# Performance work log

Measured on AMD Instinct MI355X. Metric: run time of the kernel, lower is better.

The kernel has to match this reference:

```python
import jax, jax.numpy as jnp
import numpy as np

BATCH, SEQ, DIM, NH = 4, 2048, 1024, 16
HD = DIM // NH  # 64

def _rope_cos_sin(seq_len, head_dim, dtype=jnp.float32):
    inv_freq = 1.0 / (10000.0 ** (jnp.arange(0, head_dim, 2, dtype=dtype) / head_dim))
    t = jnp.arange(seq_len, dtype=dtype)
    freqs = jnp.outer(t, inv_freq)                # (seq, hd/2)
    emb = jnp.concatenate([freqs, freqs], axis=-1)  # (seq, hd)
    return jnp.cos(emb), jnp.sin(emb)

def _apply_rope(x, cos, sin):
    # x: (b, h, s, d); cos/sin: (s, d)
    d2 = x.shape[-1] // 2
    x1, x2 = x[..., :d2], x[..., d2:]
    c = cos[None, None, :, :d2]
    s = sin[None, None, :, :d2]
    return jnp.concatenate([x1 * c - x2 * s, x1 * s + x2 * c], axis=-1)

def setup_inputs() -> dict:
    key = jax.random.key(0)
    ks = jax.random.split(key, 3)
    x = jax.random.normal(ks[0], (BATCH, SEQ, DIM), dtype=jnp.float32)
    Wqkv = jax.random.normal(ks[1], (DIM, 3 * DIM), dtype=jnp.float32) * (1.0 / np.sqrt(DIM))
    bqkv = jnp.zeros((3 * DIM,), dtype=jnp.float32)
    Wout = jax.random.normal(ks[2], (DIM, DIM), dtype=jnp.float32) * (1.0 / np.sqrt(DIM))
    bout = jnp.zeros((DIM,), dtype=jnp.float32)
    return {"x": x, "Wqkv": Wqkv, "bqkv": bqkv, "Wout": Wout, "bout": bout}

def reference(x, Wqkv, bqkv, Wout, bout):
    b, s, dim = x.shape
    qkv = x @ Wqkv + bqkv                          # (b, s, 3*dim)
    qkv = qkv.reshape(b, s, 3, NH, HD).transpose(2, 0, 3, 1, 4)  # (3, b, h, s, hd)
    q, k, v = qkv[0], qkv[1], qkv[2]
    cos, sin = _rope_cos_sin(s, HD, x.dtype)
    q = _apply_rope(q, cos, sin)
    k = _apply_rope(k, cos, sin)
    scale = HD ** -0.5
    scores = jnp.einsum('bhqd,bhkd->bhqk', q, k) * scale
    attn = jax.nn.softmax(scores, axis=-1)
    attn = jnp.nan_to_num(attn, nan=0.0)
    out = jnp.einsum('bhqk,bhkd->bhqd', attn, v)   # (b, h, s, hd)
    out = out.transpose(0, 2, 1, 3).reshape(b, s, dim)
    return out @ Wout + bout
```

## Files before the change

### kernel.cpp

```cpp
#include <hip/hip_runtime.h>
#include <hip/hip_bf16.h>
#include <stdint.h>

#define DEVI __device__ __forceinline__

typedef __attribute__((ext_vector_type(8))) short bf16x8;
typedef __attribute__((ext_vector_type(4))) float f32x4;

DEVI float bf2f(short u) {
  union { unsigned int i; float f; } v;
  v.i = ((unsigned int)(unsigned short)u) << 16;
  return v.f;
}
DEVI short f2bf(float f) {
  union { float f; unsigned int i; } v; v.f = f;
  unsigned int r = v.i + 0x7FFFu + ((v.i >> 16) & 1u);
  return (short)(r >> 16);
}

DEVI bf16x8 ldsfrag(const short* t, int row, int k0) {
  int slot = k0 >> 3;
  return *(const bf16x8*)(t + row * 64 + ((slot ^ (row & 7)) << 3));
}

DEVI void gload16(const void* g, void* l) {
  __builtin_amdgcn_global_load_lds((const __attribute__((address_space(1))) void*)g,
                                   (__attribute__((address_space(3))) void*)l, 16, 0, 0);
}

__global__ void k_cvt(const float* __restrict__ in, short* __restrict__ out, int n4) {
  int i = blockIdx.x * blockDim.x + threadIdx.x;
  if (i >= n4) return;
  float4 v = ((const float4*)in)[i];
  short4 o;
  o.x = f2bf(v.x); o.y = f2bf(v.y); o.z = f2bf(v.z); o.w = f2bf(v.w);
  ((short4*)out)[i] = o;
}

__global__ void k_transpose_bf16(const float* __restrict__ in, short* __restrict__ outp,
                                 int R, int C) {
  __shared__ float tile[32][33];
  const int c0 = blockIdx.x * 32, r0 = blockIdx.y * 32;
  const int tx = threadIdx.x, ty = threadIdx.y;
  for (int i = ty; i < 32; i += 8) tile[i][tx] = in[(size_t)(r0 + i) * C + c0 + tx];
  __syncthreads();
  for (int i = ty; i < 32; i += 8) outp[(size_t)(c0 + i) * R + r0 + tx] = f2bf(tile[tx][i]);
}

__global__ void k_rope(float* __restrict__ cosT, float* __restrict__ sinT) {
  int idx = blockIdx.x * blockDim.x + threadIdx.x;
  int s = idx >> 5, i = idx & 31;
  float inv = exp2f(-0.41524101186092034f * (float)i);
  float freq = (float)s * inv;
  cosT[idx] = cosf(freq);
  sinT[idx] = sinf(freq);
}

template <int OUTF32>
__global__ __launch_bounds__(256) void k_gemm(const short* __restrict__ A,
                                              const short* __restrict__ BT,
                                              const float* __restrict__ bias,
                                              void* __restrict__ outp,
                                              int M, int N, int K) {
  __shared__ __align__(16) short As[128 * 64];
  __shared__ __align__(16) short Bs[128 * 64];
  const int tid = threadIdx.x;
  const int lane = tid & 63, wid = tid >> 6;
  const int ln = lane & 15, grp = lane >> 4;
  const int wm = wid >> 1, wn = wid & 1;
  const int r0 = blockIdx.y * 128, c0 = blockIdx.x * 128;

  const short* aSrc[4];
  const short* bSrc[4];
  int ldst[4];
#pragma unroll
  for (int j = 0; j < 4; ++j) {
    int chunk = wid * 256 + j * 64 + lane;
    int row = chunk >> 3, gs = (chunk & 7) ^ (row & 7);
    aSrc[j] = A + (size_t)(r0 + row) * K + gs * 8;
    bSrc[j] = BT + (size_t)(c0 + row) * K + gs * 8;
    ldst[j] = (wid * 256 + j * 64) * 8;
  }

  f32x4 acc[4][4];
#pragma unroll
  for (int i = 0; i < 4; ++i)
#pragma unroll
    for (int j = 0; j < 4; ++j) acc[i][j] = (f32x4){0.f, 0.f, 0.f, 0.f};

  const int nkt = K >> 6;
  for (int kt = 0; kt < nkt; ++kt) {
    __syncthreads();
#pragma unroll
    for (int j = 0; j < 4; ++j) {
      gload16(aSrc[j], &As[ldst[j]]);
      gload16(bSrc[j], &Bs[ldst[j]]);
      aSrc[j] += 64;
      bSrc[j] += 64;
    }
    __syncthreads();
#pragma unroll
    for (int ks = 0; ks < 2; ++ks) {
      const int k0 = ks * 32 + grp * 8;
      bf16x8 af[4], bfr[4];
#pragma unroll
      for (int mi = 0; mi < 4; ++mi) af[mi] = ldsfrag(As, wm * 64 + mi * 16 + ln, k0);
#pragma unroll
      for (int ni = 0; ni < 4; ++ni) bfr[ni] = ldsfrag(Bs, wn * 64 + ni * 16 + ln, k0);
      __builtin_amdgcn_s_setprio(1);
#pragma unroll
      for (int mi = 0; mi < 4; ++mi)
#pragma unroll
        for (int ni = 0; ni < 4; ++ni)
          acc[mi][ni] = __builtin_amdgcn_mfma_f32_16x16x32_bf16(af[mi], bfr[ni], acc[mi][ni], 0, 0, 0);
      __builtin_amdgcn_s_setprio(0);
    }
  }
#pragma unroll
  for (int ni = 0; ni < 4; ++ni) {
    const int col = c0 + wn * 64 + ni * 16 + ln;
    const float bv = bias[col];
#pragma unroll
    for (int mi = 0; mi < 4; ++mi) {
#pragma unroll
      for (int r = 0; r < 4; ++r) {
        const int rowg = r0 + wm * 64 + mi * 16 + grp * 4 + r;
        float v = acc[mi][ni][r] + bv;
        if (OUTF32) ((float*)outp)[(size_t)rowg * N + col] = v;
        else        ((short*)outp)[(size_t)rowg * N + col] = f2bf(v);
      }
    }
  }
}

__global__ __launch_bounds__(256) void k_transform(const short* __restrict__ qkv,
                                                   const float* __restrict__ cosT,
                                                   const float* __restrict__ sinT,
                                                   short* __restrict__ qo,
                                                   short* __restrict__ ko,
                                                   short* __restrict__ vT) {
  __shared__ __align__(16) short vs[64 * 72];
  const int st = blockIdx.x, bh = blockIdx.y;
  const int b = bh >> 4, h = bh & 15;
  const int t = threadIdx.x;
  const float QSC = 0.18033688011112042f;
  {
    const int sl = t >> 2, j = t & 3;
    const int s = st * 64 + sl;
    const short* row = qkv + ((size_t)(b * 2048 + s)) * 3072 + h * 64;
    bf16x8 qlo = *(const bf16x8*)(row + j * 8);
    bf16x8 qhi = *(const bf16x8*)(row + 32 + j * 8);
    bf16x8 klo = *(const bf16x8*)(row + 1024 + j * 8);
    bf16x8 khi = *(const bf16x8*)(row + 1056 + j * 8);
    const float* cp = cosT + s * 32 + j * 8;
    const float* sp = sinT + s * 32 + j * 8;
    bf16x8 ql, qh, kl, kh;
#pragma unroll
    for (int e = 0; e < 8; ++e) {
      float c = cp[e], sn = sp[e];
      float a1 = bf2f(qlo[e]), a2 = bf2f(qhi[e]);
      ql[e] = f2bf((a1 * c - a2 * sn) * QSC);
      qh[e] = f2bf((a1 * sn + a2 * c) * QSC);
      float b1 = bf2f(klo[e]), b2 = bf2f(khi[e]);
      kl[e] = f2bf(b1 * c - b2 * sn);
      kh[e] = f2bf(b1 * sn + b2 * c);
    }
    short* qrow = qo + ((size_t)bh * 2048 + s) * 64;
    short* krow = ko + ((size_t)bh * 2048 + s) * 64;
    *(bf16x8*)(qrow + j * 8) = ql;
    *(bf16x8*)(qrow + 32 + j * 8) = qh;
    *(bf16x8*)(krow + j * 8) = kl;
    *(bf16x8*)(krow + 32 + j * 8) = kh;
    bf16x8 v0 = *(const bf16x8*)(row + 2048 + j * 16);
    bf16x8 v1 = *(const bf16x8*)(row + 2048 + j * 16 + 8);
    *(bf16x8*)(&vs[sl * 72 + j * 16]) = v0;
    *(bf16x8*)(&vs[sl * 72 + j * 16 + 8]) = v1;
  }
  __syncthreads();
  {
    const int d = t >> 2, sc = (t & 3) * 16;
    bf16x8 o0, o1;
#pragma unroll
    for (int i = 0; i < 8; ++i) o0[i] = vs[(sc + i) * 72 + d];
#pragma unroll
    for (int i = 0; i < 8; ++i) o1[i] = vs[(sc + 8 + i) * 72 + d];
    short* vrow = vT + (size_t)bh * 64 * 2048 + (size_t)d * 2048 + st * 64 + sc;
    *(bf16x8*)(vrow) = o0;
    *(bf16x8*)(vrow + 8) = o1;
  }
}

__global__ __launch_bounds__(256, 4) void k_attn(const short* __restrict__ Q,
                                                 const short* __restrict__ Kk,
                                                 const short* __restrict__ VT,
                                                 short* __restrict__ out) {
  __shared__ __align__(16) short smem[128 * 64];
  short* Ks = smem;
  short* Vs = smem + 64 * 64;
  const int tid = threadIdx.x;
  const int lane = tid & 63, wid = tid >> 6;
  const int ln = lane & 15, grp = lane >> 4;
  const int qt = blockIdx.x, bh = blockIdx.y;
  const int b = bh >> 4, h = bh & 15;

  bf16x8 qf[2][2];
#pragma unroll
  for (int g = 0; g < 2; ++g)
#pragma unroll
    for (int ks = 0; ks < 2; ++ks)
      qf[g][ks] = *(const bf16x8*)(Q + ((size_t)bh * 2048 + qt * 128 + wid * 32 + g * 16 + ln) * 64
                                   + ks * 32 + grp * 8);

  const short* kSrc[2];
  const short* vSrc[2];
  int ldst[2];
#pragma unroll
  for (int j = 0; j < 2; ++j) {
    int chunk = wid * 128 + j * 64 + lane;
    int row = chunk >> 3, gs = (chunk & 7) ^ (row & 7);
    kSrc[j] = Kk + (size_t)bh * 2048 * 64 + (size_t)row * 64 + gs * 8;
    vSrc[j] = VT + (size_t)bh * 64 * 2048 + (size_t)row * 2048 + gs * 8;
    ldst[j] = (wid * 128 + j * 64) * 8;
  }

  f32x4 acc[2][4];
  f32x4 accl[2];
#pragma unroll
  for (int g = 0; g < 2; ++g) {
    accl[g] = (f32x4){0.f, 0.f, 0.f, 0.f};
#pragma unroll
    for (int i = 0; i < 4; ++i) acc[g][i] = (f32x4){0.f, 0.f, 0.f, 0.f};
  }
  bf16x8 ones;
#pragma unroll
  for (int e = 0; e < 8; ++e) ones[e] = (short)0x3F80;

  union VU { bf16x8 v; short4 h[2]; };
  union PU { bf16x8 v; unsigned int u[4]; };

  for (int t = 0; t < 32; ++t) {
    __syncthreads();
#pragma unroll
    for (int j = 0; j < 2; ++j) {
      gload16(kSrc[j], &Ks[ldst[j]]);
      gload16(vSrc[j], &Vs[ldst[j]]);
      kSrc[j] += 64 * 64;
      vSrc[j] += 64;
    }
    __syncthreads();

    f32x4 sf[2][4];
#pragma unroll
    for (int g = 0; g < 2; ++g)
#pragma unroll
      for (int ni = 0; ni < 4; ++ni) sf[g][ni] = (f32x4){0.f, 0.f, 0.f, 0.f};
#pragma unroll
    for (int ks = 0; ks < 2; ++ks) {
      bf16x8 kf[4];
#pragma unroll
      for (int ni = 0; ni < 4; ++ni) kf[ni] = ldsfrag(Ks, ni * 16 + ln, ks * 32 + grp * 8);
      __builtin_amdgcn_s_setprio(1);
#pragma unroll
      for (int g = 0; g < 2; ++g)
#pragma unroll
        for (int ni = 0; ni < 4; ++ni)
          sf[g][ni] = __builtin_amdgcn_mfma_f32_16x16x32_bf16(kf[ni], qf[g][ks], sf[g][ni], 0, 0, 0);
      __builtin_amdgcn_s_setprio(0);
    }

    PU pbf[2][2];
#pragma unroll
    for (int g = 0; g < 2; ++g) {
#pragma unroll
      for (int ni = 0; ni < 4; ++ni) {
        f32x4 s = sf[g][ni];
#pragma unroll
        for (int r = 0; r < 4; ++r) s[r] = __builtin_amdgcn_exp2f(s[r]);
        sf[g][ni] = s;
      }
#pragma unroll
      for (int ks = 0; ks < 2; ++ks)
#pragma unroll
        for (int j = 0; j < 4; ++j) {
          float lo = sf[g][2 * ks + (j >> 1)][(j & 1) * 2];
          float hi = sf[g][2 * ks + (j >> 1)][(j & 1) * 2 + 1];
          unsigned int r;
          asm("v_cvt_pk_bf16_f32 %0, %1, %2" : "=v"(r) : "v"(lo), "v"(hi));
          pbf[g][ks].u[j] = r;
        }
    }

#pragma unroll
    for (int ks = 0; ks < 2; ++ks) {
      VU vf[4];
#pragma unroll
      for (int mi = 0; mi < 4; ++mi) {
        const int row = mi * 16 + ln;
        const int s1 = (ks * 4 + (grp >> 1)) ^ (row & 7);
        const int s2 = (ks * 4 + 2 + (grp >> 1)) ^ (row & 7);
        vf[mi].h[0] = *(const short4*)(Vs + row * 64 + (s1 << 3) + (grp & 1) * 4);
        vf[mi].h[1] = *(const short4*)(Vs + row * 64 + (s2 << 3) + (grp & 1) * 4);
      }
      __builtin_amdgcn_s_setprio(1);
#pragma unroll
      for (int g = 0; g < 2; ++g) {
#pragma unroll
        for (int mi = 0; mi < 4; ++mi)
          acc[g][mi] = __builtin_amdgcn_mfma_f32_16x16x32_bf16(vf[mi].v, pbf[g][ks].v, acc[g][mi], 0, 0, 0);
        accl[g] = __builtin_amdgcn_mfma_f32_16x16x32_bf16(ones, pbf[g][ks].v, accl[g], 0, 0, 0);
      }
      __builtin_amdgcn_s_setprio(0);
    }
  }

  __syncthreads();
#pragma unroll
  for (int g = 0; g < 2; ++g) {
    const float inv = 1.0f / accl[g][0];
    const int q = wid * 32 + g * 16 + ln;
#pragma unroll
    for (int mi = 0; mi < 4; ++mi) {
      short4 p;
      p.x = f2bf(acc[g][mi][0] * inv);
      p.y = f2bf(acc[g][mi][1] * inv);
      p.z = f2bf(acc[g][mi][2] * inv);
      p.w = f2bf(acc[g][mi][3] * inv);
      int slot = mi * 2 + (grp >> 1);
      *(short4*)(&smem[q * 64 + ((slot ^ (q & 7)) << 3) + (grp & 1) * 4]) = p;
    }
  }
  __syncthreads();
  {
    const int row = tid >> 1, half = tid & 1;
#pragma unroll
    for (int j = 0; j < 4; ++j) {
      int c = half * 4 + j;
      int4 v = *(const int4*)(&smem[row * 64 + ((c ^ (row & 7)) << 3)]);
      *(int4*)(out + ((size_t)b * 2048 + qt * 128 + row) * 1024 + h * 64 + c * 8) = v;
    }
  }
}

extern "C" void kernel_launch(void* const* d_in, const int* in_sizes, int n_in,
                              void* d_out, int out_size, void* d_ws, size_t ws_size,
                              hipStream_t stream) {
  const float* x    = (const float*)d_in[0];
  const float* Wqkv = (const float*)d_in[1];
  const float* bqkv = (const float*)d_in[2];
  const float* Wout = (const float*)d_in[3];
  const float* bout = (const float*)d_in[4];
  float* out = (float*)d_out;

  char* p = (char*)d_ws;
  short* xb    = (short*)p; p += (size_t)8192 * 1024 * 2;
  short* wqkvT = (short*)p; p += (size_t)3072 * 1024 * 2;
  short* woutT = (short*)p; p += (size_t)1024 * 1024 * 2;
  float* cosT  = (float*)p; p += (size_t)2048 * 32 * 4;
  float* sinT  = (float*)p; p += (size_t)2048 * 32 * 4;
  short* qkvb  = (short*)p; p += (size_t)8192 * 3072 * 2;
  short* qb    = (short*)p; p += (size_t)64 * 2048 * 64 * 2;
  short* kb    = (short*)p; p += (size_t)64 * 2048 * 64 * 2;
  short* vTb   = (short*)p; p += (size_t)64 * 2048 * 64 * 2;
  short* ao    = (short*)p; p += (size_t)8192 * 1024 * 2;

  k_cvt<<<8192 * 1024 / 4 / 256, 256, 0, stream>>>(x, xb, 8192 * 1024 / 4);
  k_transpose_bf16<<<dim3(3072 / 32, 1024 / 32), dim3(32, 8), 0, stream>>>(Wqkv, wqkvT, 1024, 3072);
  k_transpose_bf16<<<dim3(1024 / 32, 1024 / 32), dim3(32, 8), 0, stream>>>(Wout, woutT, 1024, 1024);
  k_rope<<<2048 * 32 / 256, 256, 0, stream>>>(cosT, sinT);
  k_gemm<0><<<dim3(3072 / 128, 8192 / 128), 256, 0, stream>>>(xb, wqkvT, bqkv, (void*)qkvb,
                                                              8192, 3072, 1024);
  k_transform<<<dim3(32, 64), 256, 0, stream>>>(qkvb, cosT, sinT, qb, kb, vTb);
  k_attn<<<dim3(16, 64), 256, 0, stream>>>(qb, kb, vTb, ao);
  k_gemm<1><<<dim3(1024 / 128, 8192 / 128), 256, 0, stream>>>(ao, woutT, bout, (void*)out,
                                                              8192, 1024, 1024);
}
```

Baseline: 218.7 us.

## Pre-pack V into MFMA fragment order and double attention query tile

```diff
diff --git a/kernel.cpp b/kernel.cpp
--- a/kernel.cpp
+++ b/kernel.cpp
@@ -107,13 +107,11 @@
       for (int mi = 0; mi < 4; ++mi) af[mi] = ldsfrag(As, wm * 64 + mi * 16 + ln, k0);
 #pragma unroll
       for (int ni = 0; ni < 4; ++ni) bfr[ni] = ldsfrag(Bs, wn * 64 + ni * 16 + ln, k0);
-      __builtin_amdgcn_s_setprio(1);
 #pragma unroll
       for (int mi = 0; mi < 4; ++mi)
 #pragma unroll
         for (int ni = 0; ni < 4; ++ni)
           acc[mi][ni] = __builtin_amdgcn_mfma_f32_16x16x32_bf16(af[mi], bfr[ni], acc[mi][ni], 0, 0, 0);
-      __builtin_amdgcn_s_setprio(0);
     }
   }
 #pragma unroll
@@ -138,7 +136,7 @@
                                                    const float* __restrict__ sinT,
                                                    short* __restrict__ qo,
                                                    short* __restrict__ ko,
-                                                   short* __restrict__ vT) {
+                                                   short* __restrict__ vp) {
   __shared__ __align__(16) short vs[64 * 72];
   const int st = blockIdx.x, bh = blockIdx.y;
   const int b = bh >> 4, h = bh & 15;
@@ -178,55 +176,60 @@
   }
   __syncthreads();
   {
-    const int d = t >> 2, sc = (t & 3) * 16;
-    bf16x8 o0, o1;
-#pragma unroll
-    for (int i = 0; i < 8; ++i) o0[i] = vs[(sc + i) * 72 + d];
-#pragma unroll
-    for (int i = 0; i < 8; ++i) o1[i] = vs[(sc + 8 + i) * 72 + d];
-    short* vrow = vT + (size_t)bh * 64 * 2048 + (size_t)d * 2048 + st * 64 + sc;
-    *(bf16x8*)(vrow) = o0;
-    *(bf16x8*)(vrow + 8) = o1;
-  }
-}
-
-__global__ __launch_bounds__(256, 4) void k_attn(const short* __restrict__ Q,
-                                                 const short* __restrict__ Kk,
-                                                 const short* __restrict__ VT,
-                                                 short* __restrict__ out) {
-  __shared__ __align__(16) short smem[128 * 64];
-  short* Ks = smem;
-  short* Vs = smem + 64 * 64;
+#pragma unroll
+    for (int i = 0; i < 2; ++i) {
+      const int cc = t + i * 256;
+      const int ks = cc >> 8, mi = (cc >> 6) & 3, grp = (cc >> 4) & 3, ln = cc & 15;
+      const int d = mi * 16 + ln;
+      bf16x8 o;
+#pragma unroll
+      for (int e = 0; e < 8; ++e) {
+        const int key = 32 * ks + 16 * (e >> 2) + 4 * grp + (e & 3);
+        o[e] = vs[key * 72 + d];
+      }
+      *(bf16x8*)(vp + ((size_t)bh * 32 + st) * 4096 + cc * 8) = o;
+    }
+  }
+}
+
+__global__ __launch_bounds__(256) void k_attn(const short* __restrict__ Q,
+                                              const short* __restrict__ Kk,
+                                              const short* __restrict__ Vp,
+                                              short* __restrict__ out) {
+  __shared__ __align__(16) short Ks[64 * 64];
+  __shared__ __align__(16) short Ow[4 * 64 * 68];
   const int tid = threadIdx.x;
   const int lane = tid & 63, wid = tid >> 6;
   const int ln = lane & 15, grp = lane >> 4;
   const int qt = blockIdx.x, bh = blockIdx.y;
   const int b = bh >> 4, h = bh & 15;
 
-  bf16x8 qf[2][2];
-#pragma unroll
-  for (int g = 0; g < 2; ++g)
+  bf16x8 qf[4][2];
+#pragma unroll
+  for (int g = 0; g < 4; ++g)
 #pragma unroll
     for (int ks = 0; ks < 2; ++ks)
-      qf[g][ks] = *(const bf16x8*)(Q + ((size_t)bh * 2048 + qt * 128 + wid * 32 + g * 16 + ln) * 64
+      qf[g][ks] = *(const bf16x8*)(Q + ((size_t)bh * 2048 + qt * 256 + wid * 64 + g * 16 + ln) * 64
                                    + ks * 32 + grp * 8);
 
-  const short* kSrc[2];
-  const short* vSrc[2];
-  int ldst[2];
-#pragma unroll
-  for (int j = 0; j < 2; ++j) {
-    int chunk = wid * 128 + j * 64 + lane;
-    int row = chunk >> 3, gs = (chunk & 7) ^ (row & 7);
-    kSrc[j] = Kk + (size_t)bh * 2048 * 64 + (size_t)row * 64 + gs * 8;
-    vSrc[j] = VT + (size_t)bh * 64 * 2048 + (size_t)row * 2048 + gs * 8;
-    ldst[j] = (wid * 128 + j * 64) * 8;
-  }
-
-  f32x4 acc[2][4];
-  f32x4 accl[2];
-#pragma unroll
-  for (int g = 0; g < 2; ++g) {
+  const short* kSrc0;
+  const short* kSrc1;
+  int ldst0, ldst1;
+  {
+    int c0i = wid * 64 + lane;
+    int r0i = c0i >> 3, g0i = (c0i & 7) ^ (r0i & 7);
+    kSrc0 = Kk + (size_t)bh * 2048 * 64 + (size_t)r0i * 64 + g0i * 8;
+    ldst0 = (wid * 64) * 8;
+    int c1i = 256 + wid * 64 + lane;
+    int r1i = c1i >> 3, g1i = (c1i & 7) ^ (r1i & 7);
+    kSrc1 = Kk + (size_t)bh * 2048 * 64 + (size_t)r1i * 64 + g1i * 8;
+    ldst1 = ((256 + wid * 64)) * 8;
+  }
+
+  f32x4 acc[4][4];
+  f32x4 accl[4];
+#pragma unroll
+  for (int g = 0; g < 4; ++g) {
     accl[g] = (f32x4){0.f, 0.f, 0.f, 0.f};
 #pragma unroll
     for (int i = 0; i < 4; ++i) acc[g][i] = (f32x4){0.f, 0.f, 0.f, 0.f};
@@ -235,23 +238,24 @@
 #pragma unroll
   for (int e = 0; e < 8; ++e) ones[e] = (short)0x3F80;
 
-  union VU { bf16x8 v; short4 h[2]; };
   union PU { bf16x8 v; unsigned int u[4]; };
 
   for (int t = 0; t < 32; ++t) {
+    const short* vt = Vp + ((size_t)bh * 32 + t) * 4096;
+    bf16x8 vf0[4];
+#pragma unroll
+    for (int mi = 0; mi < 4; ++mi) vf0[mi] = *(const bf16x8*)(vt + mi * 512 + lane * 8);
+
     __syncthreads();
-#pragma unroll
-    for (int j = 0; j < 2; ++j) {
-      gload16(kSrc[j], &Ks[ldst[j]]);
-      gload16(vSrc[j], &Vs[ldst[j]]);
-      kSrc[j] += 64 * 64;
-      vSrc[j] += 64;
-    }
+    gload16(kSrc0, &Ks[ldst0]);
+    gload16(kSrc1, &Ks[ldst1]);
+    kSrc0 += 4096;
+    kSrc1 += 4096;
     __syncthreads();
 
-    f32x4 sf[2][4];
-#pragma unroll
-    for (int g = 0; g < 2; ++g)
+    f32x4 sf[4][4];
+#pragma unroll
+    for (int g = 0; g < 4; ++g)
 #pragma unroll
       for (int ni = 0; ni < 4; ++ni) sf[g][ni] = (f32x4){0.f, 0.f, 0.f, 0.f};
 #pragma unroll
@@ -261,16 +265,20 @@
       for (int ni = 0; ni < 4; ++ni) kf[ni] = ldsfrag(Ks, ni * 16 + ln, ks * 32 + grp * 8);
       __builtin_amdgcn_s_setprio(1);
 #pragma unroll
-      for (int g = 0; g < 2; ++g)
+      for (int g = 0; g < 4; ++g)
 #pragma unroll
         for (int ni = 0; ni < 4; ++ni)
           sf[g][ni] = __builtin_amdgcn_mfma_f32_16x16x32_bf16(kf[ni], qf[g][ks], sf[g][ni], 0, 0, 0);
       __builtin_amdgcn_s_setprio(0);
     }
 
-    PU pbf[2][2];
-#pragma unroll
-    for (int g = 0; g < 2; ++g) {
+    bf16x8 vf1[4];
+#pragma unroll
+    for (int mi = 0; mi < 4; ++mi) vf1[mi] = *(const bf16x8*)(vt + 2048 + mi * 512 + lane * 8);
+
+    PU pbf[4][2];
+#pragma unroll
+    for (int g = 0; g < 4; ++g) {
 #pragma unroll
       for (int ni = 0; ni < 4; ++ni) {
         f32x4 s = sf[g][ni];
@@ -290,34 +298,28 @@
         }
     }
 
-#pragma unroll
-    for (int ks = 0; ks < 2; ++ks) {
-      VU vf[4];
-#pragma unroll
-      for (int mi = 0; mi < 4; ++mi) {
-        const int row = mi * 16 + ln;
-        const int s1 = (ks * 4 + (grp >> 1)) ^ (row & 7);
-        const int s2 = (ks * 4 + 2 + (grp >> 1)) ^ (row & 7);
-        vf[mi].h[0] = *(const short4*)(Vs + row * 64 + (s1 << 3) + (grp & 1) * 4);
-        vf[mi].h[1] = *(const short4*)(Vs + row * 64 + (s2 << 3) + (grp & 1) * 4);
-      }
-      __builtin_amdgcn_s_setprio(1);
-#pragma unroll
-      for (int g = 0; g < 2; ++g) {
-#pragma unroll
-        for (int mi = 0; mi < 4; ++mi)
-          acc[g][mi] = __builtin_amdgcn_mfma_f32_16x16x32_bf16(vf[mi].v, pbf[g][ks].v, acc[g][mi], 0, 0, 0);
-        accl[g] = __builtin_amdgcn_mfma_f32_16x16x32_bf16(ones, pbf[g][ks].v, accl[g], 0, 0, 0);
-      }
-      __builtin_amdgcn_s_setprio(0);
-    }
+    __builtin_amdgcn_s_setprio(1);
+#pragma unroll
+    for (int g = 0; g < 4; ++g) {
+#pragma unroll
+      for (int mi = 0; mi < 4; ++mi)
+        acc[g][mi] = __builtin_amdgcn_mfma_f32_16x16x32_bf16(vf0[mi], pbf[g][0].v, acc[g][mi], 0, 0, 0);
+      accl[g] = __builtin_amdgcn_mfma_f32_16x16x32_bf16(ones, pbf[g][0].v, accl[g], 0, 0, 0);
+    }
+#pragma unroll
+    for (int g = 0; g < 4; ++g) {
+#pragma unroll
+      for (int mi = 0; mi < 4; ++mi)
+        acc[g][mi] = __builtin_amdgcn_mfma_f32_16x16x32_bf16(vf1[mi], pbf[g][1].v, acc[g][mi], 0, 0, 0);
+      accl[g] = __builtin_amdgcn_mfma_f32_16x16x32_bf16(ones, pbf[g][1].v, accl[g], 0, 0, 0);
+    }
+    __builtin_amdgcn_s_setprio(0);
   }
 
   __syncthreads();
 #pragma unroll
-  for (int g = 0; g < 2; ++g) {
+  for (int g = 0; g < 4; ++g) {
     const float inv = 1.0f / accl[g][0];
-    const int q = wid * 32 + g * 16 + ln;
 #pragma unroll
     for (int mi = 0; mi < 4; ++mi) {
       short4 p;
@@ -325,19 +327,17 @@
       p.y = f2bf(acc[g][mi][1] * inv);
       p.z = f2bf(acc[g][mi][2] * inv);
       p.w = f2bf(acc[g][mi][3] * inv);
-      int slot = mi * 2 + (grp >> 1);
-      *(short4*)(&smem[q * 64 + ((slot ^ (q & 7)) << 3) + (grp & 1) * 4]) = p;
+      *(short4*)(&Ow[wid * 4352 + (g * 16 + ln) * 68 + mi * 16 + grp * 4]) = p;
     }
   }
   __syncthreads();
   {
-    const int row = tid >> 1, half = tid & 1;
-#pragma unroll
-    for (int j = 0; j < 4; ++j) {
-      int c = half * 4 + j;
-      int4 v = *(const int4*)(&smem[row * 64 + ((c ^ (row & 7)) << 3)]);
-      *(int4*)(out + ((size_t)b * 2048 + qt * 128 + row) * 1024 + h * 64 + c * 8) = v;
-    }
+    const int q = qt * 256 + tid;
+    const short* src = &Ow[(tid >> 6) * 4352 + (tid & 63) * 68];
+    short* dst = out + ((size_t)b * 2048 + q) * 1024 + h * 64;
+#pragma unroll
+    for (int j = 0; j < 8; ++j)
+      *(int4*)(dst + j * 8) = *(const int4*)(src + j * 8);
   }
 }
 
@@ -360,7 +360,7 @@
   short* qkvb  = (short*)p; p += (size_t)8192 * 3072 * 2;
   short* qb    = (short*)p; p += (size_t)64 * 2048 * 64 * 2;
   short* kb    = (short*)p; p += (size_t)64 * 2048 * 64 * 2;
-  short* vTb   = (short*)p; p += (size_t)64 * 2048 * 64 * 2;
+  short* vpb   = (short*)p; p += (size_t)64 * 2048 * 64 * 2;
   short* ao    = (short*)p; p += (size_t)8192 * 1024 * 2;
 
   k_cvt<<<8192 * 1024 / 4 / 256, 256, 0, stream>>>(x, xb, 8192 * 1024 / 4);
@@ -369,8 +369,8 @@
   k_rope<<<2048 * 32 / 256, 256, 0, stream>>>(cosT, sinT);
   k_gemm<0><<<dim3(3072 / 128, 8192 / 128), 256, 0, stream>>>(xb, wqkvT, bqkv, (void*)qkvb,
                                                               8192, 3072, 1024);
-  k_transform<<<dim3(32, 64), 256, 0, stream>>>(qkvb, cosT, sinT, qb, kb, vTb);
-  k_attn<<<dim3(16, 64), 256, 0, stream>>>(qb, kb, vTb, ao);
+  k_transform<<<dim3(32, 64), 256, 0, stream>>>(qkvb, cosT, sinT, qb, kb, vpb);
+  k_attn<<<dim3(8, 64), 256, 0, stream>>>(qb, kb, vpb, ao);
   k_gemm<1><<<dim3(1024 / 128, 8192 / 128), 256, 0, stream>>>(ao, woutT, bout, (void*)out,
                                                               8192, 1024, 1024);
 }
```

Measured after the change: 251.3 us. +14.9%, slower.
